# Optimization experiments

Measured on AMD Instinct MI355X. Metric: run time of the kernel, lower is better.

Reference implementation:

```python
import jax, jax.numpy as jnp
from jax import lax
import numpy as np

B, T, D, H, DH, FF, K = 16, 1024, 512, 8, 64, 2048, 3
EPS = 1e-5


def _layer_norm(x, g, b):
    mu = jnp.mean(x, axis=-1, keepdims=True)
    var = jnp.mean((x - mu) ** 2, axis=-1, keepdims=True)
    return (x - mu) / jnp.sqrt(var + EPS) * g + b


def setup_inputs() -> dict:
    key = jax.random.key(0)
    ks = jax.random.split(key, 14)
    f32 = jnp.float32
    dec_inp = jax.random.normal(ks[0], (B, T, D), f32)
    lengths = jax.random.randint(ks[1], (B,), T // 2, T + 1)
    mask = (jnp.arange(T)[None, :] < lengths[:, None])[:, :, None]  # [B,T,1] bool
    qkv_w = jax.random.normal(ks[2], (3 * H * DH, D), f32) * (D ** -0.5)
    qkv_b = jnp.zeros((3 * H * DH,), f32)
    o_w = jax.random.normal(ks[3], (D, H * DH), f32) * ((H * DH) ** -0.5)
    ln1_g = jnp.ones((D,), f32)
    ln1_b = jnp.zeros((D,), f32)
    conv1_w = jax.random.normal(ks[4], (FF, D, K), f32) * ((D * K) ** -0.5)
    conv1_b = jnp.zeros((FF,), f32)
    conv2_w = jax.random.normal(ks[5], (D, FF, K), f32) * ((FF * K) ** -0.5)
    conv2_b = jnp.zeros((D,), f32)
    ln2_g = jnp.ones((D,), f32)
    ln2_b = jnp.zeros((D,), f32)
    return dict(dec_inp=dec_inp, mask=mask, qkv_w=qkv_w, qkv_b=qkv_b, o_w=o_w,
                ln1_g=ln1_g, ln1_b=ln1_b, conv1_w=conv1_w, conv1_b=conv1_b,
                conv2_w=conv2_w, conv2_b=conv2_b, ln2_g=ln2_g, ln2_b=ln2_b)


def reference(dec_inp, mask, qkv_w, qkv_b, o_w, ln1_g, ln1_b,
              conv1_w, conv1_b, conv2_w, conv2_b, ln2_g, ln2_b):
    # ----- MultiHeadAttn (post-norm, dropout = identity in eval) -----
    attn_mask = ~mask[:, :, 0]                      # [B,T], True = pad
    qkv = dec_inp @ qkv_w.T + qkv_b                 # [B,T,3*H*DH]
    q, k, v = jnp.split(qkv, 3, axis=2)

    def to_heads(x):  # [B,T,H*DH] -> [B*H,T,DH] (batch-major, as in torch)
        return x.reshape(B, T, H, DH).transpose(0, 2, 1, 3).reshape(B * H, T, DH)

    q, k, v = to_heads(q), to_heads(k), to_heads(v)
    scores = jnp.einsum('bqd,bkd->bqk', q, k) * (DH ** -0.5)  # [B*H,T,T]
    # faithful to torch: mask tiled head-major (index i % B)
    am = jnp.tile(attn_mask[:, None, :], (H, T, 1))           # [B*H,T,T]
    scores = jnp.where(am, -jnp.inf, scores)
    prob = jax.nn.softmax(scores, axis=2)
    vec = jnp.einsum('bqk,bkd->bqd', prob, v)                 # [B*H,T,DH]
    # faithful to torch: view as [H,B,...] then permute
    vec = vec.reshape(H, B, T, DH).transpose(1, 2, 0, 3).reshape(B, T, H * DH)
    attn_out = vec @ o_w.T                                    # [B,T,D]
    out = _layer_norm(dec_inp + attn_out, ln1_g, ln1_b)
    out = out * mask

    # ----- PositionwiseConvFF (post-norm) -----
    x = out.transpose(0, 2, 1)                                # [B,D,T]
    h = lax.conv_general_dilated(x, conv1_w, (1,), [(K // 2, K // 2)],
                                 dimension_numbers=('NCH', 'OIH', 'NCH'))
    h = jax.nn.relu(h + conv1_b[None, :, None])
    h = lax.conv_general_dilated(h, conv2_w, (1,), [(K // 2, K // 2)],
                                 dimension_numbers=('NCH', 'OIH', 'NCH'))
    core = (h + conv2_b[None, :, None]).transpose(0, 2, 1)    # [B,T,D]
    out = _layer_norm(out + core, ln2_g, ln2_b)
    return out * mask
```

## Files before the change

kernel.cpp:

```cpp
#include <hip/hip_runtime.h>

using h16 = _Float16;
using h16x4 = __attribute__((ext_vector_type(4))) _Float16;
using h16x8 = __attribute__((ext_vector_type(8))) _Float16;
using f32x4 = __attribute__((ext_vector_type(4))) float;

static constexpr int cB = 16, cT = 1024, cD = 512, cH = 8, cDH = 64, cFF = 2048;
static constexpr int cM = cB * cT;
static constexpr int cTP = cT + 2;

__device__ __forceinline__ bool mask_val(const void* mb, int idx) {
  const unsigned char* u8 = (const unsigned char*)mb;
  if (u8[1] == 1) return u8[idx] != 0;
  const float* f = (const float*)mb;
  if (f[1] == 1.0f) return f[idx] != 0.0f;
  return ((const int*)mb)[idx] != 0;
}

__device__ __forceinline__ void gl_lds16(const h16* g, h16* l) {
  __builtin_amdgcn_global_load_lds(
      (const __attribute__((address_space(1))) unsigned int*)g,
      (__attribute__((address_space(3))) unsigned int*)l, 16, 0, 0);
}


__global__ __launch_bounds__(256) void k_cast4(const float* __restrict__ in,
                                               h16* __restrict__ out, int n4) {
  int i = blockIdx.x * 256 + threadIdx.x;
  if (i >= n4) return;
  const float4 f = ((const float4*)in)[i];
  h16x4 o = {(h16)f.x, (h16)f.y, (h16)f.z, (h16)f.w};
  ((h16x4*)out)[i] = o;
}

__global__ __launch_bounds__(256) void k_repack_w1(const float* __restrict__ w,
                                                   h16* __restrict__ out) {
  int i = blockIdx.x * 256 + threadIdx.x;
  if (i >= cFF * cD) return;
  int f = i >> 9, d = i & 511;
#pragma unroll
  for (int k = 0; k < 3; ++k)
    out[f * (3 * cD) + k * cD + d] = (h16)w[(long)i * 3 + k];
}

__global__ __launch_bounds__(256) void k_repack_w2(const float* __restrict__ w,
                                                   h16* __restrict__ out) {
  int i = blockIdx.x * 256 + threadIdx.x;
  if (i >= cD * cFF) return;
  int o = i >> 11, f = i & 2047;
#pragma unroll
  for (int k = 0; k < 3; ++k)
    out[o * (3 * cFF) + k * cFF + f] = (h16)w[(long)i * 3 + k];
}

__global__ __launch_bounds__(256) void k_zero_pads(h16* __restrict__ xp,
                                                   h16* __restrict__ hp) {
  int i = blockIdx.x * 256 + threadIdx.x;
  if (i < cB * 2 * cD) {
    int b = i / (2 * cD); int rr = (i / cD) & 1; int c = i % cD;
    xp[((long)b * cTP + rr * (cTP - 1)) * cD + c] = (h16)0.f;
  }
  if (i < cB * 2 * cFF) {
    int b = i / (2 * cFF); int rr = (i / cFF) & 1; int c = i % cFF;
    hp[((long)b * cTP + rr * (cTP - 1)) * cFF + c] = (h16)0.f;
  }
}

template <int SKIP, bool A_CONV, bool OUT_CONV, bool BIAS, bool RELU,
          bool OUT_H16, bool VSCAT, int SPLITK, bool SWIZ>
__global__ __launch_bounds__(256)
void gemm_bt(const h16* __restrict__ A, const h16* __restrict__ W,
             const float* __restrict__ bias, void* __restrict__ Cv,
             h16* __restrict__ Vg, const void* __restrict__ maskbuf,
             int ldc, int Kd, int lda, long zstride) {
  __shared__ h16 smem[2 * 128 * 64];
  h16* As = smem;
  h16* Bs = smem + 128 * 64;
  const int tid = threadIdx.x;
  const int w = tid >> 6, l = tid & 63;
  int m0, n0;
  if (SWIZ) {
    m0 = (blockIdx.x * 16 + (blockIdx.y >> 2)) * 128;
    n0 = (blockIdx.y & 3) * 128;
  } else {
    m0 = blockIdx.y * 128;
    n0 = blockIdx.x * 128;
  }

  if (SKIP == 1) {
    if (!mask_val(maskbuf, m0)) return;
  } else if (SKIP == 2) {
    int t0 = m0 & 1023, base = ((m0 >> 10) & 1) * 8;
    bool need = false;
#pragma unroll
    for (int i = 0; i < 8; ++i) need |= mask_val(maskbuf, ((base + i) << 10) + t0);
    if (!need) return;
  } else if (SKIP == 3) {
    int t0 = m0 & 1023;
    if (t0 && !mask_val(maskbuf, m0 - 1)) return;
  }

  const int wm = (w >> 1) * 64, wn = (w & 1) * 64;
  const int lr = l >> 3;
  const int lcs = ((l & 7) ^ lr) * 8;
  const int fr = l & 15;
  const int fb = fr & 7;
  const int qd = l >> 4;

  const int kspan = (SPLITK == 2) ? (Kd >> 1) : Kd;
  const int kbeg = (SPLITK == 2) ? blockIdx.z * kspan : 0;
  const int kend = kbeg + kspan;

  f32x4 zero4 = {0.f, 0.f, 0.f, 0.f};
  f32x4 acc[4][4];
#pragma unroll
  for (int mi = 0; mi < 4; ++mi)
#pragma unroll
    for (int ni = 0; ni < 4; ++ni) acc[mi][ni] = zero4;

  for (int k0 = kbeg; k0 < kend; k0 += 64) {
    __syncthreads();
#pragma unroll
    for (int i = 0; i < 4; ++i) {
      int c = w * 4 + i;
      int ar = m0 + c * 8 + lr;
      long aoff = (long)(ar + (A_CONV ? 2 * (ar >> 10) : 0)) * lda + k0 + lcs;
      gl_lds16(A + aoff, &As[c * 512]);
      int br = n0 + c * 8 + lr;
      long boff = (long)br * Kd + k0 + lcs;
      gl_lds16(W + boff, &Bs[c * 512]);
    }
    __syncthreads();
#pragma unroll
    for (int kc = 0; kc < 2; ++kc) {
      h16x8 af[4], bfr[4];
#pragma unroll
      for (int mi = 0; mi < 4; ++mi)
        af[mi] = *(const h16x8*)&As[(wm + mi * 16 + fr) * 64 +
                                    (((kc * 4 + qd) ^ fb) * 8)];
#pragma unroll
      for (int ni = 0; ni < 4; ++ni)
        bfr[ni] = *(const h16x8*)&Bs[(wn + ni * 16 + fr) * 64 +
                                     (((kc * 4 + qd) ^ fb) * 8)];
#pragma unroll
      for (int mi = 0; mi < 4; ++mi)
#pragma unroll
        for (int ni = 0; ni < 4; ++ni)
          acc[mi][ni] = __builtin_amdgcn_mfma_f32_16x16x32_f16(
              af[mi], bfr[ni], acc[mi][ni], 0, 0, 0);
    }
  }
  const bool do_bias = BIAS && (SPLITK == 1 || blockIdx.z == 0);
  if (VSCAT && n0 >= 1024) {
#pragma unroll
    for (int mi = 0; mi < 4; ++mi) {
      int t0 = (m0 + wm + mi * 16 + (l >> 4) * 4) & 1023;
      int jj = ((m0 >> 10) << 3);
#pragma unroll
      for (int ni = 0; ni < 4; ++ni) {
        int gc = n0 + wn + ni * 16 + fr;
        int dh = gc & 63;
        int j2 = jj + ((gc - 1024) >> 6);
        float bb = do_bias ? bias[gc] : 0.f;
        h16x4 v4 = {(h16)(acc[mi][ni][0] + bb), (h16)(acc[mi][ni][1] + bb),
                    (h16)(acc[mi][ni][2] + bb), (h16)(acc[mi][ni][3] + bb)};
        *(h16x4*)&Vg[((long)j2 * 64 + dh) * 1024 + t0] = v4;
      }
    }
  } else if (OUT_H16) {
    __syncthreads();
#pragma unroll
    for (int mi = 0; mi < 4; ++mi) {
#pragma unroll
      for (int ni = 0; ni < 4; ++ni) {
#pragma unroll
        for (int rr = 0; rr < 4; ++rr) {
          int rrow = wm + mi * 16 + (l >> 4) * 4 + rr;
          int ccol = wn + ni * 16 + fr;
          float v = acc[mi][ni][rr];
          if (do_bias) v += bias[n0 + ccol];
          if (RELU) v = v > 0.f ? v : 0.f;
          smem[rrow * 128 + ccol] = (h16)v;
        }
      }
    }
    __syncthreads();
    h16* outp = (h16*)Cv + (SPLITK == 2 ? (long)blockIdx.z * zstride : 0);
    const int r2 = tid >> 4, c2 = (tid & 15) * 8;
#pragma unroll
    for (int i = 0; i < 8; ++i) {
      int row = r2 + i * 16;
      int gr = m0 + row;
      long orow = (long)gr + (OUT_CONV ? (2 * (gr >> 10) + 1) : 0);
      *(h16x8*)&outp[orow * ldc + n0 + c2] = *(h16x8*)&smem[row * 128 + c2];
    }
  } else {
#pragma unroll
    for (int mi = 0; mi < 4; ++mi) {
#pragma unroll
      for (int ni = 0; ni < 4; ++ni) {
#pragma unroll
        for (int rr = 0; rr < 4; ++rr) {
          int gr = m0 + wm + mi * 16 + (l >> 4) * 4 + rr;
          int gc = n0 + wn + ni * 16 + fr;
          float v = acc[mi][ni][rr];
          if (do_bias) v += bias[gc];
          if (RELU) v = v > 0.f ? v : 0.f;
          long orow = (long)gr + (OUT_CONV ? (2 * (gr >> 10) + 1) : 0);
          ((float*)Cv)[orow * ldc + gc] = v;
        }
      }
    }
  }
}

template <int SKIP, bool A_CONV, bool OUT_CONV, bool BIAS, bool RELU,
          int SPLITK, int NBLK_LOG2>
__global__ __launch_bounds__(512, 2)
void gemm8(const h16* __restrict__ A, const h16* __restrict__ W,
           const float* __restrict__ bias, h16* __restrict__ C,
           const void* __restrict__ maskbuf, int ldc, int Kd, int lda,
           long zstride) {
  extern __shared__ h16 sm[];
  const int tid = threadIdx.x;
  const int wid = tid >> 6, l = tid & 63;
  const int m0 = (blockIdx.x * 8 + (blockIdx.y >> NBLK_LOG2)) * 256;
  const int n0 = (blockIdx.y & ((1 << NBLK_LOG2) - 1)) * 256;

  if (SKIP == 1) {
    if (!mask_val(maskbuf, m0)) return;
  } else if (SKIP == 3) {
    int t0 = m0 & 1023;
    if (t0 && !mask_val(maskbuf, m0 - 1)) return;
  }

  const int wm = wid >> 2, wn = wid & 3;
  const int fr = l & 15, qd = l >> 4, fb = fr & 7;
  const int lr = l >> 3;
  const int lcs = ((l & 7) ^ lr) * 8;

  const int kspan = (SPLITK == 2) ? (Kd >> 1) : Kd;
  const int kbeg = (SPLITK == 2) ? blockIdx.z * kspan : 0;
  const int nt = kspan >> 6;

  f32x4 zero4 = {0.f, 0.f, 0.f, 0.f};
  f32x4 acc[8][4];
#pragma unroll
  for (int m = 0; m < 8; ++m)
#pragma unroll
    for (int n = 0; n < 4; ++n) acc[m][n] = zero4;

  auto stage = [&](int ti, h16* Ab, h16* Bb) {
#pragma unroll
    for (int i = 0; i < 4; ++i) {
      int c = wid * 4 + i;
      int ar = m0 + c * 8 + lr;
      long aoff = (long)(ar + (A_CONV ? 2 * (ar >> 10) : 0)) * lda +
                  kbeg + ti * 64 + lcs;
      gl_lds16(A + aoff, &Ab[c * 512]);
      int br = n0 + c * 8 + lr;
      long boff = (long)br * Kd + kbeg + ti * 64 + lcs;
      gl_lds16(W + boff, &Bb[c * 512]);
    }
  };

  stage(0, sm, sm + 16384);
  stage(1, sm + 32768, sm + 49152);
  asm volatile("s_waitcnt vmcnt(8)" ::: "memory");
  __builtin_amdgcn_s_barrier();

  const int arow = wm * 128 + fr;
  const int brow = wn * 64 + fr;
  const int sA = (qd ^ fb) * 8;
  const int sB = ((4 + qd) ^ fb) * 8;

  for (int t = 0; t < nt; ++t) {
    h16* Ab = sm + (t & 1) * 32768;
    h16* Bb = Ab + 16384;
    h16x8 a0[8], b0[4];
#pragma unroll
    for (int m = 0; m < 8; ++m)
      a0[m] = *(const h16x8*)&Ab[(arow + m * 16) * 64 + sA];
#pragma unroll
    for (int n = 0; n < 4; ++n)
      b0[n] = *(const h16x8*)&Bb[(brow + n * 16) * 64 + sA];
    __builtin_amdgcn_s_setprio(1);
#pragma unroll
    for (int m = 0; m < 8; ++m)
#pragma unroll
      for (int n = 0; n < 4; ++n)
        acc[m][n] = __builtin_amdgcn_mfma_f32_16x16x32_f16(a0[m], b0[n],
                                                           acc[m][n], 0, 0, 0);
    __builtin_amdgcn_s_setprio(0);
    h16x8 a1[8], b1[4];
#pragma unroll
    for (int m = 0; m < 8; ++m)
      a1[m] = *(const h16x8*)&Ab[(arow + m * 16) * 64 + sB];
#pragma unroll
    for (int n = 0; n < 4; ++n)
      b1[n] = *(const h16x8*)&Bb[(brow + n * 16) * 64 + sB];
    asm volatile("s_waitcnt lgkmcnt(0)" ::: "memory");
    __builtin_amdgcn_s_barrier();
    const bool pf = (t + 2 < nt);
    if (pf) stage(t + 2, Ab, Bb);
    __builtin_amdgcn_s_setprio(1);
#pragma unroll
    for (int m = 0; m < 8; ++m)
#pragma unroll
      for (int n = 0; n < 4; ++n)
        acc[m][n] = __builtin_amdgcn_mfma_f32_16x16x32_f16(a1[m], b1[n],
                                                           acc[m][n], 0, 0, 0);
    __builtin_amdgcn_s_setprio(0);
    if (t + 1 < nt) {
      if (pf)
        asm volatile("s_waitcnt vmcnt(8)" ::: "memory");
      else
        asm volatile("s_waitcnt vmcnt(0)" ::: "memory");
      __builtin_amdgcn_s_barrier();
    }
  }

  const bool do_bias = BIAS && (SPLITK == 1 || blockIdx.z == 0);
  const int qd4 = qd * 4;
#pragma unroll
  for (int m = 0; m < 8; ++m) {
    int row = wm * 128 + m * 16 + qd4;
#pragma unroll
    for (int n = 0; n < 4; ++n) {
      int col = wn * 64 + n * 16 + fr;
      float bb = do_bias ? bias[n0 + col] : 0.f;
#pragma unroll
      for (int rr = 0; rr < 4; ++rr) {
        float v = acc[m][n][rr] + bb;
        if (RELU) v = v > 0.f ? v : 0.f;
        sm[(row + rr) * 256 + col] = (h16)v;
      }
    }
  }
  __syncthreads();
  h16* outp = C + (SPLITK == 2 ? (long)blockIdx.z * zstride : 0);
  const int r2 = tid >> 5, c2 = (tid & 31) * 8;
#pragma unroll
  for (int i = 0; i < 16; ++i) {
    int row = r2 + i * 16;
    int gr = m0 + row;
    long orow = (long)gr + (OUT_CONV ? (2 * (gr >> 10) + 1) : 0);
    *(h16x8*)&outp[orow * (long)ldc + n0 + c2] = *(h16x8*)&sm[row * 256 + c2];
  }
}

__global__ __launch_bounds__(256)
void k_attn(const h16* __restrict__ qk, const h16* __restrict__ Vg,
            const void* __restrict__ maskbuf, h16* __restrict__ attn_out) {
  __shared__ h16 Ks[64 * 64];
  __shared__ h16 Vt[64 * 64];
  __shared__ h16 Ps[4][16 * 68];
  __shared__ float sbias[64];
  const int tid = threadIdx.x, w = tid >> 6, l = tid & 63;
  const int f = blockIdx.x;
  const int bp = f & 15, qt = (f >> 4) & 15, hp = f >> 8;
  const int j = hp * 16 + bp;
  const int bd = j >> 3, hd = j & 7;

  if (!mask_val(maskbuf, bp * cT + qt * 64)) return;

  const int fr = l & 15, fq = (l >> 4) * 8;
  const int fb = fr & 7, qd = l >> 4;
  const int lr = l >> 3, lcs = ((l & 7) ^ lr) * 8;

  h16x8 qf[2];
#pragma unroll
  for (int kc = 0; kc < 2; ++kc) {
    qf[kc] = *(const h16x8*)&qk[
        (long)((bd << 10) + qt * 64 + w * 16 + fr) * 1024 +
        hd * 64 + kc * 32 + fq];
    qf[kc] *= (h16)0.125f;
  }

  f32x4 zero4 = {0.f, 0.f, 0.f, 0.f};
  f32x4 o[4];
  float lrow[4];
#pragma unroll
  for (int nt = 0; nt < 4; ++nt) o[nt] = zero4;
#pragma unroll
  for (int r = 0; r < 4; ++r) lrow[r] = 0.f;

  for (int k0 = 0; k0 < cT; k0 += 64) {
    if (!mask_val(maskbuf, bp * cT + k0)) break;
    __syncthreads();
#pragma unroll
    for (int i = 0; i < 2; ++i) {
      int c = w * 2 + i;
      int row = c * 8 + lr;
      gl_lds16(qk + (long)((bd << 10) + k0 + row) * 1024 + 512 + hd * 64 + lcs,
               &Ks[c * 512]);
      gl_lds16(Vg + ((long)j * 64 + row) * 1024 + k0 + lcs, &Vt[c * 512]);
    }
    if (tid < 64)
      sbias[tid] = mask_val(maskbuf, bp * cT + k0 + tid) ? 0.f : -1e30f;
    __syncthreads();

    f32x4 S[4];
#pragma unroll
    for (int kt = 0; kt < 4; ++kt) {
      float sb = sbias[kt * 16 + fr];
      f32x4 s = {sb, sb, sb, sb};
#pragma unroll
      for (int kc = 0; kc < 2; ++kc) {
        h16x8 kf = *(const h16x8*)&Ks[(kt * 16 + fr) * 64 +
                                      (((kc * 4 + qd) ^ fb) * 8)];
        s = __builtin_amdgcn_mfma_f32_16x16x32_f16(qf[kc], kf, s, 0, 0, 0);
      }
      S[kt] = s;
    }
#pragma unroll
    for (int r = 0; r < 4; ++r) {
      float p0 = __expf(S[0][r] - 4.f), p1 = __expf(S[1][r] - 4.f);
      float p2 = __expf(S[2][r] - 4.f), p3 = __expf(S[3][r] - 4.f);
      lrow[r] += (p0 + p1) + (p2 + p3);
      int ql = (l >> 4) * 4 + r;
      Ps[w][ql * 68 + fr] = (h16)p0;
      Ps[w][ql * 68 + 16 + fr] = (h16)p1;
      Ps[w][ql * 68 + 32 + fr] = (h16)p2;
      Ps[w][ql * 68 + 48 + fr] = (h16)p3;
    }
#pragma unroll
    for (int kp = 0; kp < 2; ++kp) {
      h16x8 pf = *(const h16x8*)&Ps[w][fr * 68 + kp * 32 + fq];
#pragma unroll
      for (int nt = 0; nt < 4; ++nt) {
        h16x8 vf = *(const h16x8*)&Vt[(nt * 16 + fr) * 64 +
                                      (((kp * 4 + qd) ^ fb) * 8)];
        o[nt] = __builtin_amdgcn_mfma_f32_16x16x32_f16(pf, vf, o[nt], 0, 0, 0);
      }
    }
  }
#pragma unroll
  for (int r = 0; r < 4; ++r) {
#pragma unroll
    for (int m = 1; m < 16; m <<= 1) lrow[r] += __shfl_xor(lrow[r], m);
    float inv = 1.f / lrow[r];
    int q = qt * 64 + w * 16 + (l >> 4) * 4 + r;
    long row = (long)bp * cT + q;
#pragma unroll
    for (int nt = 0; nt < 4; ++nt)
      attn_out[row * cD + hp * 64 + nt * 16 + fr] = (h16)(o[nt][r] * inv);
  }
}

template <bool WRITE_XP, bool RH16, bool R2H16>
__global__ __launch_bounds__(256)
void k_ln(const float* __restrict__ X, const void* __restrict__ Rv,
          const void* __restrict__ Rv2,
          const float* __restrict__ g, const float* __restrict__ bta,
          const void* __restrict__ maskbuf,
          float* __restrict__ outf, h16* __restrict__ xp) {
  const int w = threadIdx.x >> 6, l = threadIdx.x & 63;
  const long row = (long)blockIdx.x * 4 + w;
  const float4* x4 = (const float4*)(X + row * cD);
  float4 a0 = x4[l], a1 = x4[l + 64];
  float v[8];
  if (RH16) {
    const h16x4* r4 = (const h16x4*)((const h16*)Rv + row * cD);
    h16x4 b0 = r4[l], b1 = r4[l + 64];
    v[0] = a0.x + (float)b0[0]; v[1] = a0.y + (float)b0[1];
    v[2] = a0.z + (float)b0[2]; v[3] = a0.w + (float)b0[3];
    v[4] = a1.x + (float)b1[0]; v[5] = a1.y + (float)b1[1];
    v[6] = a1.z + (float)b1[2]; v[7] = a1.w + (float)b1[3];
  } else {
    const float4* r4 = (const float4*)((const float*)Rv + row * cD);
    float4 b0 = r4[l], b1 = r4[l + 64];
    v[0] = a0.x + b0.x; v[1] = a0.y + b0.y; v[2] = a0.z + b0.z; v[3] = a0.w + b0.w;
    v[4] = a1.x + b1.x; v[5] = a1.y + b1.y; v[6] = a1.z + b1.z; v[7] = a1.w + b1.w;
  }
  if (R2H16) {
    const h16x4* r4 = (const h16x4*)((const h16*)Rv2 + row * cD);
    h16x4 b0 = r4[l], b1 = r4[l + 64];
    v[0] += (float)b0[0]; v[1] += (float)b0[1];
    v[2] += (float)b0[2]; v[3] += (float)b0[3];
    v[4] += (float)b1[0]; v[5] += (float)b1[1];
    v[6] += (float)b1[2]; v[7] += (float)b1[3];
  }
  float s = 0.f;
#pragma unroll
  for (int i = 0; i < 8; ++i) s += v[i];
#pragma unroll
  for (int m = 1; m < 64; m <<= 1) s += __shfl_xor(s, m);
  const float mu = s * (1.f / 512.f);
  float s2 = 0.f;
#pragma unroll
  for (int i = 0; i < 8; ++i) { float d = v[i] - mu; s2 += d * d; }
#pragma unroll
  for (int m = 1; m < 64; m <<= 1) s2 += __shfl_xor(s2, m);
  const float rstd = rsqrtf(s2 * (1.f / 512.f) + 1e-5f);
  const float mv = mask_val(maskbuf, (int)row) ? 1.f : 0.f;
  const float4* g4 = (const float4*)g;
  const float4* t4 = (const float4*)bta;
  float4 g0 = g4[l], g1 = g4[l + 64], t0 = t4[l], t1 = t4[l + 64];
  float4 y0, y1;
  y0.x = ((v[0] - mu) * rstd * g0.x + t0.x) * mv;
  y0.y = ((v[1] - mu) * rstd * g0.y + t0.y) * mv;
  y0.z = ((v[2] - mu) * rstd * g0.z + t0.z) * mv;
  y0.w = ((v[3] - mu) * rstd * g0.w + t0.w) * mv;
  y1.x = ((v[4] - mu) * rstd * g1.x + t1.x) * mv;
  y1.y = ((v[5] - mu) * rstd * g1.y + t1.y) * mv;
  y1.z = ((v[6] - mu) * rstd * g1.z + t1.z) * mv;
  y1.w = ((v[7] - mu) * rstd * g1.w + t1.w) * mv;
  ((float4*)(outf + row * cD))[l] = y0;
  ((float4*)(outf + row * cD))[l + 64] = y1;
  if (WRITE_XP) {
    const long xrow = row + 2 * (row >> 10) + 1;
    h16x4 h0 = {(h16)y0.x, (h16)y0.y, (h16)y0.z, (h16)y0.w};
    h16x4 h1 = {(h16)y1.x, (h16)y1.y, (h16)y1.z, (h16)y1.w};
    ((h16x4*)(xp + xrow * cD))[l] = h0;
    ((h16x4*)(xp + xrow * cD))[l + 64] = h1;
  }
}

extern "C" void kernel_launch(void* const* d_in, const int* in_sizes, int n_in,
                              void* d_out, int out_size, void* d_ws, size_t ws_size,
                              hipStream_t stream) {
  const float* dec   = (const float*)d_in[0];
  const void*  maskb = d_in[1];
  const float* qkv_w = (const float*)d_in[2];
  const float* qkv_b = (const float*)d_in[3];
  const float* o_w   = (const float*)d_in[4];
  const float* ln1g  = (const float*)d_in[5];
  const float* ln1b  = (const float*)d_in[6];
  const float* c1w   = (const float*)d_in[7];
  const float* c1b   = (const float*)d_in[8];
  const float* c2w   = (const float*)d_in[9];
  const float* c2b   = (const float*)d_in[10];
  const float* ln2g  = (const float*)d_in[11];
  const float* ln2b  = (const float*)d_in[12];

  char* p = (char*)d_ws;
  auto alloc = [&](size_t bytes) {
    char* r = p; p += (bytes + 255) & ~(size_t)255; return r;
  };
  h16*   dec_h  = (h16*)alloc((size_t)cM * cD * 2);
  h16*   qkvw_h = (h16*)alloc((size_t)1536 * cD * 2);
  h16*   ow_h   = (h16*)alloc((size_t)cD * cD * 2);
  h16*   w1p    = (h16*)alloc((size_t)cFF * 3 * cD * 2);
  h16*   w2p    = (h16*)alloc((size_t)cD * 3 * cFF * 2);
  h16*   qk_h   = (h16*)alloc((size_t)cM * 1024 * 2);
  h16*   vg     = (h16*)alloc((size_t)cB * cH * cDH * cT * 2);
  h16*   attn_h = (h16*)alloc((size_t)cM * cD * 2);
  float* tmp    = (float*)alloc((size_t)cM * cD * 4);
  float* out1   = (float*)alloc((size_t)cM * cD * 4);
  h16*   xp     = (h16*)alloc((size_t)cB * cTP * cD * 2);
  h16*   hp     = (h16*)alloc((size_t)cB * cTP * cFF * 2);
  h16*   core0 = attn_h;
  h16*   core1 = qk_h;
  (void)ws_size; (void)n_in; (void)in_sizes; (void)out_size;

  static bool s_attr = false;
  if (!s_attr) {
    hipFuncSetAttribute(
        reinterpret_cast<const void*>(&gemm8<3, true, true, true, true, 1, 3>),
        hipFuncAttributeMaxDynamicSharedMemorySize, 131072);
    hipFuncSetAttribute(
        reinterpret_cast<const void*>(&gemm8<1, true, false, true, false, 2, 1>),
        hipFuncAttributeMaxDynamicSharedMemorySize, 131072);
    s_attr = true;
  }

  k_cast4<<<(cM * cD / 4 + 255) / 256, 256, 0, stream>>>(dec, dec_h, cM * cD / 4);
  k_cast4<<<(1536 * cD / 4 + 255) / 256, 256, 0, stream>>>(qkv_w, qkvw_h, 1536 * cD / 4);
  k_cast4<<<(cD * cD / 4 + 255) / 256, 256, 0, stream>>>(o_w, ow_h, cD * cD / 4);
  k_repack_w1<<<(cFF * cD + 255) / 256, 256, 0, stream>>>(c1w, w1p);
  k_repack_w2<<<(cD * cFF + 255) / 256, 256, 0, stream>>>(c2w, w2p);
  k_zero_pads<<<(cB * 2 * cFF + 255) / 256, 256, 0, stream>>>(xp, hp);

  gemm_bt<2, false, false, true, false, true, true, 1, false>
      <<<dim3(12, cM / 128), 256, 0, stream>>>(dec_h, qkvw_h, qkv_b, qk_h, vg,
                                               maskb, 1024, cD, cD, 0);

  k_attn<<<dim3(2048), 256, 0, stream>>>(qk_h, vg, maskb, attn_h);

  gemm_bt<1, false, false, false, false, false, false, 1, false>
      <<<dim3(cD / 128, cM / 128), 256, 0, stream>>>(attn_h, ow_h, nullptr, tmp,
                                                     nullptr, maskb, cD, cD, cD, 0);

  k_ln<true, false, false><<<cM / 4, 256, 0, stream>>>(dec, tmp, nullptr, ln1g,
                                                       ln1b, maskb, out1, xp);

  gemm8<3, true, true, true, true, 1, 3>
      <<<dim3(8, 64), dim3(512), 131072, stream>>>(xp, w1p, c1b, hp, maskb,
                                                   cFF, 3 * cD, cD, 0);

  gemm8<1, true, false, true, false, 2, 1>
      <<<dim3(8, 16, 2), dim3(512), 131072, stream>>>(hp, w2p, c2b, core0,
                                                      maskb, cD, 3 * cFF, cFF,
                                                      (long)(core1 - core0));

  k_ln<false, true, true><<<cM / 4, 256, 0, stream>>>(out1, core0, core1, ln2g,
                                                      ln2b, maskb,
                                                      (float*)d_out, nullptr);
}
```

Measured before the change: 501.5 us.

## Restructure GEMM main loop into four-phase ping-pong with split A/B staging

The GEMM inner loop is split into four MFMA phases, each covering half of the M tiles and half of the K slice. LDS reads for the next phase and the global-to-LDS prefetches (A and B staged separately) are interleaved between phases, with extra barriers and sched_barriers. The aim is to overlap LDS reads and global loads with MFMA work and to lower register pressure by keeping fewer fragments live at once. In exchange it adds many more workgroup barriers per iteration, and the interleaved reads and writes to the shared buffers carry a risk of race hazards.

After: 500.9 us. Within noise of the previous version (-0.1%).

```diff
diff --git a/kernel.cpp b/kernel.cpp
--- a/kernel.cpp
+++ b/kernel.cpp
@@ -250,7 +250,8 @@
 #pragma unroll
     for (int n = 0; n < 4; ++n) acc[m][n] = zero4;
 
-  auto stage = [&](int ti, h16* Ab, h16* Bb) {
+  auto stageA = [&](int ti) {
+    h16* Ab = sm + (ti & 1) * 32768;
 #pragma unroll
     for (int i = 0; i < 4; ++i) {
       int c = wid * 4 + i;
@@ -258,66 +259,121 @@
       long aoff = (long)(ar + (A_CONV ? 2 * (ar >> 10) : 0)) * lda +
                   kbeg + ti * 64 + lcs;
       gl_lds16(A + aoff, &Ab[c * 512]);
+    }
+  };
+  auto stageB = [&](int ti) {
+    h16* Bb = sm + (ti & 1) * 32768 + 16384;
+#pragma unroll
+    for (int i = 0; i < 4; ++i) {
+      int c = wid * 4 + i;
       int br = n0 + c * 8 + lr;
       long boff = (long)br * Kd + kbeg + ti * 64 + lcs;
       gl_lds16(W + boff, &Bb[c * 512]);
     }
   };
-
-  stage(0, sm, sm + 16384);
-  stage(1, sm + 32768, sm + 49152);
-  asm volatile("s_waitcnt vmcnt(8)" ::: "memory");
-  __builtin_amdgcn_s_barrier();
 
   const int arow = wm * 128 + fr;
   const int brow = wn * 64 + fr;
   const int sA = (qd ^ fb) * 8;
   const int sB = ((4 + qd) ^ fb) * 8;
 
-  for (int t = 0; t < nt; ++t) {
-    h16* Ab = sm + (t & 1) * 32768;
-    h16* Bb = Ab + 16384;
-    h16x8 a0[8], b0[4];
-#pragma unroll
-    for (int m = 0; m < 8; ++m)
-      a0[m] = *(const h16x8*)&Ab[(arow + m * 16) * 64 + sA];
+  h16x8 a0A[4], a0B[4], a1A[4], a1B[4], b0[4], b1[4];
+
+  stageA(0); stageB(0);
+  if (nt > 1) stageB(1);
+  asm volatile("s_waitcnt vmcnt(4)" ::: "memory");
+  __builtin_amdgcn_s_barrier();
+  {
+    const h16* Ab = sm;
+    const h16* Bb = sm + 16384;
+#pragma unroll
+    for (int i = 0; i < 4; ++i)
+      a0A[i] = *(const h16x8*)&Ab[(arow + i * 16) * 64 + sA];
 #pragma unroll
     for (int n = 0; n < 4; ++n)
       b0[n] = *(const h16x8*)&Bb[(brow + n * 16) * 64 + sA];
+    if (nt > 1) stageA(1);
+  }
+
+  for (int t = 0; t < nt; ++t) {
+    const h16* Ab = sm + (t & 1) * 32768;
+    const h16* Bb = Ab + 16384;
+#pragma unroll
+    for (int i = 0; i < 4; ++i)
+      a0B[i] = *(const h16x8*)&Ab[(arow + i * 16) * 64 + sB];
+#pragma unroll
+    for (int n = 0; n < 4; ++n)
+      b1[n] = *(const h16x8*)&Bb[(brow + n * 16) * 64 + sB];
+    __builtin_amdgcn_s_barrier();
+    asm volatile("s_waitcnt lgkmcnt(0)" ::: "memory");
+    __builtin_amdgcn_sched_barrier(0);
     __builtin_amdgcn_s_setprio(1);
 #pragma unroll
-    for (int m = 0; m < 8; ++m)
+    for (int m = 0; m < 4; ++m)
 #pragma unroll
       for (int n = 0; n < 4; ++n)
-        acc[m][n] = __builtin_amdgcn_mfma_f32_16x16x32_f16(a0[m], b0[n],
+        acc[m][n] = __builtin_amdgcn_mfma_f32_16x16x32_f16(a0A[m], b0[n],
                                                            acc[m][n], 0, 0, 0);
     __builtin_amdgcn_s_setprio(0);
-    h16x8 a1[8], b1[4];
-#pragma unroll
-    for (int m = 0; m < 8; ++m)
-      a1[m] = *(const h16x8*)&Ab[(arow + m * 16) * 64 + sB];
-#pragma unroll
-    for (int n = 0; n < 4; ++n)
-      b1[n] = *(const h16x8*)&Bb[(brow + n * 16) * 64 + sB];
+    __builtin_amdgcn_s_barrier();
+#pragma unroll
+    for (int i = 0; i < 4; ++i)
+      a1A[i] = *(const h16x8*)&Ab[(arow + (4 + i) * 16) * 64 + sA];
+    if (t + 2 < nt) stageB(t + 2);
+    __builtin_amdgcn_s_barrier();
     asm volatile("s_waitcnt lgkmcnt(0)" ::: "memory");
-    __builtin_amdgcn_s_barrier();
-    const bool pf = (t + 2 < nt);
-    if (pf) stage(t + 2, Ab, Bb);
+    __builtin_amdgcn_sched_barrier(0);
     __builtin_amdgcn_s_setprio(1);
 #pragma unroll
-    for (int m = 0; m < 8; ++m)
+    for (int m = 0; m < 4; ++m)
 #pragma unroll
       for (int n = 0; n < 4; ++n)
-        acc[m][n] = __builtin_amdgcn_mfma_f32_16x16x32_f16(a1[m], b1[n],
+        acc[m][n] = __builtin_amdgcn_mfma_f32_16x16x32_f16(a0B[m], b1[n],
                                                            acc[m][n], 0, 0, 0);
     __builtin_amdgcn_s_setprio(0);
+    __builtin_amdgcn_s_barrier();
+#pragma unroll
+    for (int i = 0; i < 4; ++i)
+      a1B[i] = *(const h16x8*)&Ab[(arow + (4 + i) * 16) * 64 + sB];
+    __builtin_amdgcn_s_barrier();
+    asm volatile("s_waitcnt lgkmcnt(0)" ::: "memory");
+    __builtin_amdgcn_sched_barrier(0);
+    __builtin_amdgcn_s_setprio(1);
+#pragma unroll
+    for (int m = 0; m < 4; ++m)
+#pragma unroll
+      for (int n = 0; n < 4; ++n)
+        acc[4 + m][n] = __builtin_amdgcn_mfma_f32_16x16x32_f16(
+            a1A[m], b0[n], acc[4 + m][n], 0, 0, 0);
+    __builtin_amdgcn_s_setprio(0);
+    if (t + 2 < nt)
+      asm volatile("s_waitcnt vmcnt(4)" ::: "memory");
+    else
+      asm volatile("s_waitcnt vmcnt(0)" ::: "memory");
+    __builtin_amdgcn_s_barrier();
     if (t + 1 < nt) {
-      if (pf)
-        asm volatile("s_waitcnt vmcnt(8)" ::: "memory");
-      else
-        asm volatile("s_waitcnt vmcnt(0)" ::: "memory");
-      __builtin_amdgcn_s_barrier();
-    }
+      const h16* Ab1 = sm + ((t + 1) & 1) * 32768;
+      const h16* Bb1 = Ab1 + 16384;
+#pragma unroll
+      for (int i = 0; i < 4; ++i)
+        a0A[i] = *(const h16x8*)&Ab1[(arow + i * 16) * 64 + sA];
+#pragma unroll
+      for (int n = 0; n < 4; ++n)
+        b0[n] = *(const h16x8*)&Bb1[(brow + n * 16) * 64 + sA];
+      if (t + 2 < nt) stageA(t + 2);
+    }
+    __builtin_amdgcn_s_barrier();
+    asm volatile("s_waitcnt lgkmcnt(0)" ::: "memory");
+    __builtin_amdgcn_sched_barrier(0);
+    __builtin_amdgcn_s_setprio(1);
+#pragma unroll
+    for (int m = 0; m < 4; ++m)
+#pragma unroll
+      for (int n = 0; n < 4; ++n)
+        acc[4 + m][n] = __builtin_amdgcn_mfma_f32_16x16x32_f16(
+            a1B[m], b1[n], acc[4 + m][n], 0, 0, 0);
+    __builtin_amdgcn_s_setprio(0);
+    __builtin_amdgcn_s_barrier();
   }
 
   const bool do_bias = BIAS && (SPLITK == 1 || blockIdx.z == 0);
```

## Split 256x256 conv GEMM tile across 16 waves instead of 8

Applied to the files above, without the earlier changes.

Doubles the block size of the conv-FFN GEMM from 512 to 1024 threads, so each of 16 waves computes a 64x64 sub-tile instead of 128x64. The accumulator count per wave halves, and staging and epilogue work are split across twice as many threads. The intent is to cut register pressure and give more waves to hide LDS and global-load latency. In exchange, there are more barriers per k-step among more waves, and the launch bound of 4 blocks per SM with 1024 threads is unlikely to be achievable given 128KB of shared memory per block.

Result: faster. 487.7 us (-2.7%).

```diff
diff --git a/kernel.cpp b/kernel.cpp
--- a/kernel.cpp
+++ b/kernel.cpp
@@ -216,11 +216,11 @@
 
 template <int SKIP, bool A_CONV, bool OUT_CONV, bool BIAS, bool RELU,
           int SPLITK, int NBLK_LOG2>
-__global__ __launch_bounds__(512, 2)
-void gemm8(const h16* __restrict__ A, const h16* __restrict__ W,
-           const float* __restrict__ bias, h16* __restrict__ C,
-           const void* __restrict__ maskbuf, int ldc, int Kd, int lda,
-           long zstride) {
+__global__ __launch_bounds__(1024, 4)
+void gemm16(const h16* __restrict__ A, const h16* __restrict__ W,
+            const float* __restrict__ bias, h16* __restrict__ C,
+            const void* __restrict__ maskbuf, int ldc, int Kd, int lda,
+            long zstride) {
   extern __shared__ h16 sm[];
   const int tid = threadIdx.x;
   const int wid = tid >> 6, l = tid & 63;
@@ -244,16 +244,18 @@
   const int nt = kspan >> 6;
 
   f32x4 zero4 = {0.f, 0.f, 0.f, 0.f};
-  f32x4 acc[8][4];
-#pragma unroll
-  for (int m = 0; m < 8; ++m)
+  f32x4 acc[4][4];
+#pragma unroll
+  for (int m = 0; m < 4; ++m)
 #pragma unroll
     for (int n = 0; n < 4; ++n) acc[m][n] = zero4;
 
-  auto stage = [&](int ti, h16* Ab, h16* Bb) {
-#pragma unroll
-    for (int i = 0; i < 4; ++i) {
-      int c = wid * 4 + i;
+  auto stage = [&](int ti) {
+    h16* Ab = sm + (ti & 1) * 32768;
+    h16* Bb = Ab + 16384;
+#pragma unroll
+    for (int i = 0; i < 2; ++i) {
+      int c = wid * 2 + i;
       int ar = m0 + c * 8 + lr;
       long aoff = (long)(ar + (A_CONV ? 2 * (ar >> 10) : 0)) * lda +
                   kbeg + ti * 64 + lcs;
@@ -264,67 +266,65 @@
     }
   };
 
-  stage(0, sm, sm + 16384);
-  stage(1, sm + 32768, sm + 49152);
-  asm volatile("s_waitcnt vmcnt(8)" ::: "memory");
-  __builtin_amdgcn_s_barrier();
-
-  const int arow = wm * 128 + fr;
+  const int arow = wm * 64 + fr;
   const int brow = wn * 64 + fr;
   const int sA = (qd ^ fb) * 8;
   const int sB = ((4 + qd) ^ fb) * 8;
 
+  stage(0);
+  if (nt > 1) stage(1);
+  asm volatile("s_waitcnt vmcnt(4)" ::: "memory");
+  __builtin_amdgcn_s_barrier();
+
   for (int t = 0; t < nt; ++t) {
-    h16* Ab = sm + (t & 1) * 32768;
-    h16* Bb = Ab + 16384;
-    h16x8 a0[8], b0[4];
-#pragma unroll
-    for (int m = 0; m < 8; ++m)
-      a0[m] = *(const h16x8*)&Ab[(arow + m * 16) * 64 + sA];
+    const h16* Ab = sm + (t & 1) * 32768;
+    const h16* Bb = Ab + 16384;
+    const bool pf = (t + 2 < nt);
+    h16x8 a[4], b[4];
+#pragma unroll
+    for (int m = 0; m < 4; ++m)
+      a[m] = *(const h16x8*)&Ab[(arow + m * 16) * 64 + sA];
 #pragma unroll
     for (int n = 0; n < 4; ++n)
-      b0[n] = *(const h16x8*)&Bb[(brow + n * 16) * 64 + sA];
+      b[n] = *(const h16x8*)&Bb[(brow + n * 16) * 64 + sA];
     __builtin_amdgcn_s_setprio(1);
 #pragma unroll
-    for (int m = 0; m < 8; ++m)
+    for (int m = 0; m < 4; ++m)
 #pragma unroll
       for (int n = 0; n < 4; ++n)
-        acc[m][n] = __builtin_amdgcn_mfma_f32_16x16x32_f16(a0[m], b0[n],
+        acc[m][n] = __builtin_amdgcn_mfma_f32_16x16x32_f16(a[m], b[n],
                                                            acc[m][n], 0, 0, 0);
     __builtin_amdgcn_s_setprio(0);
-    h16x8 a1[8], b1[4];
-#pragma unroll
-    for (int m = 0; m < 8; ++m)
-      a1[m] = *(const h16x8*)&Ab[(arow + m * 16) * 64 + sB];
+    h16x8 a2[4], b2[4];
+#pragma unroll
+    for (int m = 0; m < 4; ++m)
+      a2[m] = *(const h16x8*)&Ab[(arow + m * 16) * 64 + sB];
 #pragma unroll
     for (int n = 0; n < 4; ++n)
-      b1[n] = *(const h16x8*)&Bb[(brow + n * 16) * 64 + sB];
+      b2[n] = *(const h16x8*)&Bb[(brow + n * 16) * 64 + sB];
     asm volatile("s_waitcnt lgkmcnt(0)" ::: "memory");
     __builtin_amdgcn_s_barrier();
-    const bool pf = (t + 2 < nt);
-    if (pf) stage(t + 2, Ab, Bb);
+    if (pf) stage(t + 2);
     __builtin_amdgcn_s_setprio(1);
 #pragma unroll
-    for (int m = 0; m < 8; ++m)
+    for (int m = 0; m < 4; ++m)
 #pragma unroll
       for (int n = 0; n < 4; ++n)
-        acc[m][n] = __builtin_amdgcn_mfma_f32_16x16x32_f16(a1[m], b1[n],
+        acc[m][n] = __builtin_amdgcn_mfma_f32_16x16x32_f16(a2[m], b2[n],
                                                            acc[m][n], 0, 0, 0);
     __builtin_amdgcn_s_setprio(0);
-    if (t + 1 < nt) {
-      if (pf)
-        asm volatile("s_waitcnt vmcnt(8)" ::: "memory");
-      else
-        asm volatile("s_waitcnt vmcnt(0)" ::: "memory");
-      __builtin_amdgcn_s_barrier();
-    }
+    if (pf)
+      asm volatile("s_waitcnt vmcnt(4)" ::: "memory");
+    else
+      asm volatile("s_waitcnt vmcnt(0)" ::: "memory");
+    __builtin_amdgcn_s_barrier();
   }
 
   const bool do_bias = BIAS && (SPLITK == 1 || blockIdx.z == 0);
   const int qd4 = qd * 4;
 #pragma unroll
-  for (int m = 0; m < 8; ++m) {
-    int row = wm * 128 + m * 16 + qd4;
+  for (int m = 0; m < 4; ++m) {
+    int row = wm * 64 + m * 16 + qd4;
 #pragma unroll
     for (int n = 0; n < 4; ++n) {
       int col = wn * 64 + n * 16 + fr;
@@ -341,8 +341,8 @@
   h16* outp = C + (SPLITK == 2 ? (long)blockIdx.z * zstride : 0);
   const int r2 = tid >> 5, c2 = (tid & 31) * 8;
 #pragma unroll
-  for (int i = 0; i < 16; ++i) {
-    int row = r2 + i * 16;
+  for (int i = 0; i < 8; ++i) {
+    int row = r2 + i * 32;
     int gr = m0 + row;
     long orow = (long)gr + (OUT_CONV ? (2 * (gr >> 10) + 1) : 0);
     *(h16x8*)&outp[orow * (long)ldc + n0 + c2] = *(h16x8*)&sm[row * 256 + c2];
@@ -557,10 +557,10 @@
   static bool s_attr = false;
   if (!s_attr) {
     hipFuncSetAttribute(
-        reinterpret_cast<const void*>(&gemm8<3, true, true, true, true, 1, 3>),
+        reinterpret_cast<const void*>(&gemm16<3, true, true, true, true, 1, 3>),
         hipFuncAttributeMaxDynamicSharedMemorySize, 131072);
     hipFuncSetAttribute(
-        reinterpret_cast<const void*>(&gemm8<1, true, false, true, false, 2, 1>),
+        reinterpret_cast<const void*>(&gemm16<1, true, false, true, false, 2, 1>),
         hipFuncAttributeMaxDynamicSharedMemorySize, 131072);
     s_attr = true;
   }
@@ -585,14 +585,14 @@
   k_ln<true, false, false><<<cM / 4, 256, 0, stream>>>(dec, tmp, nullptr, ln1g,
                                                        ln1b, maskb, out1, xp);
 
-  gemm8<3, true, true, true, true, 1, 3>
-      <<<dim3(8, 64), dim3(512), 131072, stream>>>(xp, w1p, c1b, hp, maskb,
-                                                   cFF, 3 * cD, cD, 0);
-
-  gemm8<1, true, false, true, false, 2, 1>
-      <<<dim3(8, 16, 2), dim3(512), 131072, stream>>>(hp, w2p, c2b, core0,
-                                                      maskb, cD, 3 * cFF, cFF,
-                                                      (long)(core1 - core0));
+  gemm16<3, true, true, true, true, 1, 3>
+      <<<dim3(8, 64), dim3(1024), 131072, stream>>>(xp, w1p, c1b, hp, maskb,
+                                                    cFF, 3 * cD, cD, 0);
+
+  gemm16<1, true, false, true, false, 2, 1>
+      <<<dim3(8, 16, 2), dim3(1024), 131072, stream>>>(hp, w2p, c2b, core0,
+                                                       maskb, cD, 3 * cFF, cFF,
+                                                       (long)(core1 - core0));
 
   k_ln<false, true, true><<<cM / 4, 256, 0, stream>>>(out1, core0, core1, ln2g,
                                                       ln2b, maskb,
```
